# Optimization experiments

Measured on AMD Instinct MI355X. Metric: run time of the kernel, lower is better.

Reference implementation:

```python
import jax, jax.numpy as jnp
import numpy as np

V, H, L, NH, I, S, B, T = 30522, 768, 12, 12, 3072, 512, 16, 2
DH = H // NH
EPS = 1e-12


def layer_norm(x, w, b):
    u = x.mean(-1, keepdims=True)
    s = ((x - u) ** 2).mean(-1, keepdims=True)
    return w * (x - u) / jnp.sqrt(s + EPS) + b


def setup_inputs() -> dict:
    key = jax.random.key(0)
    ks = jax.random.split(key, 32)
    std = 0.02
    inp = {
        "input_ids": jax.random.randint(ks[0], (B, S), 0, V),
        "token_type_ids": jax.random.randint(ks[1], (B, S), 0, T),
        "attention_mask": jnp.ones((B, S), jnp.float32),
        "word_emb": std * jax.random.normal(ks[2], (V, H), jnp.float32),
        "pos_emb": std * jax.random.normal(ks[3], (S, H), jnp.float32),
        "type_emb": std * jax.random.normal(ks[4], (T, H), jnp.float32),
        "emb_ln_w": jnp.ones((H,), jnp.float32),
        "emb_ln_b": jnp.zeros((H,), jnp.float32),
        # stacked per-layer params, layout [L, in, out] for x @ W + b
        "Wq": std * jax.random.normal(ks[5], (L, H, H), jnp.float32),
        "bq": jnp.zeros((L, H), jnp.float32),
        "Wk": std * jax.random.normal(ks[6], (L, H, H), jnp.float32),
        "bk": jnp.zeros((L, H), jnp.float32),
        "Wv": std * jax.random.normal(ks[7], (L, H, H), jnp.float32),
        "bv": jnp.zeros((L, H), jnp.float32),
        "Wo": std * jax.random.normal(ks[8], (L, H, H), jnp.float32),
        "bo": jnp.zeros((L, H), jnp.float32),
        "ln1_w": jnp.ones((L, H), jnp.float32),
        "ln1_b": jnp.zeros((L, H), jnp.float32),
        "W1": std * jax.random.normal(ks[9], (L, H, I), jnp.float32),
        "b1": jnp.zeros((L, I), jnp.float32),
        "W2": std * jax.random.normal(ks[10], (L, I, H), jnp.float32),
        "b2": jnp.zeros((L, H), jnp.float32),
        "ln2_w": jnp.ones((L, H), jnp.float32),
        "ln2_b": jnp.zeros((L, H), jnp.float32),
    }
    return inp


def bert_forward(input_ids, token_type_ids, attention_mask,
                 word_emb, pos_emb, type_emb, emb_ln_w, emb_ln_b,
                 Wq, bq, Wk, bk, Wv, bv, Wo, bo, ln1_w, ln1_b,
                 W1, b1, W2, b2, ln2_w, ln2_b):
    b, s = input_ids.shape
    # extended attention mask: (1 - mask) * -10000, broadcast [B,1,1,S]
    ext_mask = ((1.0 - attention_mask) * -10000.0)[:, None, None, :]

    x = word_emb[input_ids] + pos_emb[None, :s] + type_emb[token_type_ids]
    x = layer_norm(x, emb_ln_w, emb_ln_b)  # [B,S,H]

    def block(h, p):
        (wq, bq_, wk, bk_, wv, bv_, wo, bo_, l1w, l1b, w1, b1_, w2, b2_, l2w, l2b) = p
        def heads(y):  # [B,S,H] -> [B,NH,S,DH]
            return y.reshape(b, s, NH, DH).transpose(0, 2, 1, 3)
        q = heads(h @ wq + bq_)
        k = heads(h @ wk + bk_)
        v = heads(h @ wv + bv_)
        scores = jnp.einsum("bhqd,bhkd->bhqk", q, k) / jnp.sqrt(jnp.float32(DH))
        scores = scores + ext_mask
        probs = jax.nn.softmax(scores, axis=-1)
        ctx = jnp.einsum("bhqk,bhkd->bhqd", probs, v)
        ctx = ctx.transpose(0, 2, 1, 3).reshape(b, s, H)
        attn_out = ctx @ wo + bo_
        h = layer_norm(attn_out + h, l1w, l1b)
        ffn = jax.nn.gelu(h @ w1 + b1_, approximate=False) @ w2 + b2_
        h = layer_norm(ffn + h, l2w, l2b)
        return h, None

    params = (Wq, bq, Wk, bk, Wv, bv, Wo, bo, ln1_w, ln1_b, W1, b1, W2, b2, ln2_w, ln2_b)
    x, _ = jax.lax.scan(block, x, params)
    return x


def reference(input_ids, token_type_ids, attention_mask,
              word_emb, pos_emb, type_emb, emb_ln_w, emb_ln_b,
              Wq, bq, Wk, bk, Wv, bv, Wo, bo, ln1_w, ln1_b,
              W1, b1, W2, b2, ln2_w, ln2_b):
    return bert_forward(input_ids, token_type_ids, attention_mask,
                        word_emb, pos_emb, type_emb, emb_ln_w, emb_ln_b,
                        Wq, bq, Wk, bk, Wv, bv, Wo, bo, ln1_w, ln1_b,
                        W1, b1, W2, b2, ln2_w, ln2_b)
```

## Files before the change

### kernel.cpp

```cpp
#include <hip/hip_runtime.h>
#include <math.h>

typedef unsigned short u16;
typedef __bf16 bf16x8 __attribute__((ext_vector_type(8)));
typedef float f32x4 __attribute__((ext_vector_type(4)));
typedef unsigned short u16x8 __attribute__((ext_vector_type(8)));

__device__ __forceinline__ u16 f2b(float f) {
    union { float f; unsigned int u; } v; v.f = f;
    unsigned int u = v.u;
    u += 0x7fffu + ((u >> 16) & 1u);
    return (u16)(u >> 16);
}

__device__ __forceinline__ f32x4 mfma16(bf16x8 a, bf16x8 b, f32x4 c) {
    return __builtin_amdgcn_mfma_f32_16x16x32_bf16(a, b, c, 0, 0, 0);
}

__device__ __forceinline__ void g2l16(const u16* g, const u16* l) {
    __builtin_amdgcn_global_load_lds(
        reinterpret_cast<const __attribute__((address_space(1))) unsigned int*>(
            reinterpret_cast<uintptr_t>(g)),
        reinterpret_cast<__attribute__((address_space(3))) unsigned int*>(
            reinterpret_cast<uintptr_t>(l)),
        16, 0, 0);
}

__global__ __launch_bounds__(256) void transpose_all(
    const float* __restrict__ Wq, const float* __restrict__ Wk,
    const float* __restrict__ Wv, const float* __restrict__ Wo,
    const float* __restrict__ W1, const float* __restrict__ W2,
    u16* __restrict__ out) {
    int bid = blockIdx.x;
    int layer = bid / 1728;
    int w = bid % 1728;
    const float* src; u16* dst; int K, N, tid;
    u16* lbase = out + (size_t)layer * 7077888;
    if (w < 576) {
        int m = w / 144; tid = w % 144; K = 768; N = 768;
        const float* s4[4] = {Wq, Wk, Wv, Wo};
        src = s4[m] + (size_t)layer * 589824;
        dst = lbase + (size_t)m * 589824;
    } else if (w < 1152) {
        tid = w - 576; K = 768; N = 3072;
        src = W1 + (size_t)layer * 2359296;
        dst = lbase + 2359296;
    } else {
        tid = w - 1152; K = 3072; N = 768;
        src = W2 + (size_t)layer * 2359296;
        dst = lbase + 4718592;
    }
    int ntn = N >> 6;
    int tk = tid / ntn, tn = tid % ntn;
    int k0 = tk << 6, n0 = tn << 6;
    __shared__ float tile[64][68];
    int t = threadIdx.x;
    int tx4 = (t & 15) * 4, r = t >> 4;
#pragma unroll
    for (int i = 0; i < 4; i++) {
        int row = r + i * 16;
        *(f32x4*)&tile[row][tx4] =
            *(const f32x4*)&src[(size_t)(k0 + row) * N + n0 + tx4];
    }
    __syncthreads();
#pragma unroll
    for (int i = 0; i < 2; i++) {
        int idx = t + i * 256;
        int n = idx & 63, kk = (idx >> 6) * 8;
        u16x8 o;
#pragma unroll
        for (int j = 0; j < 8; j++) o[j] = f2b(tile[kk + j][n]);
        *(u16x8*)&dst[(size_t)(n0 + n) * K + k0 + kk] = o;
    }
}

__global__ __launch_bounds__(256) void pack_bias(
    const float* __restrict__ bq, const float* __restrict__ bk,
    const float* __restrict__ bv, float* __restrict__ out) {
    int i = blockIdx.x * 256 + threadIdx.x;
    if (i < 12 * 2304) {
        int l = i / 2304, r = i % 2304;
        float v = (r < 768) ? bq[l * 768 + r]
                : (r < 1536) ? bk[l * 768 + r - 768]
                             : bv[l * 768 + r - 1536];
        out[i] = v;
    }
}

__device__ __forceinline__ void block_red2(float& a, float& b, float* red) {
#pragma unroll
    for (int mk = 1; mk < 64; mk <<= 1) {
        a += __shfl_xor(a, mk, 64);
        b += __shfl_xor(b, mk, 64);
    }
    int w = threadIdx.x >> 6;
    if ((threadIdx.x & 63) == 0) { red[w * 2] = a; red[w * 2 + 1] = b; }
    __syncthreads();
    a = red[0] + red[2] + red[4] + red[6];
    b = red[1] + red[3] + red[5] + red[7];
}

__global__ __launch_bounds__(256) void embed_ln(
    const int* __restrict__ ids, const int* __restrict__ tts,
    const float* __restrict__ we, const float* __restrict__ pe,
    const float* __restrict__ te, const float* __restrict__ lw,
    const float* __restrict__ lb, float* __restrict__ x, u16* __restrict__ xb) {
    int tok = blockIdx.x, t = threadIdx.x;
    int s = tok & 511;
    size_t wrow = (size_t)ids[tok] * 768;
    size_t trow = (size_t)tts[tok] * 768;
    __shared__ float red[8];
    float e[3], sum = 0.f, sq = 0.f;
#pragma unroll
    for (int i = 0; i < 3; i++) {
        int j = i * 256 + t;
        e[i] = we[wrow + j] + pe[(size_t)s * 768 + j] + te[trow + j];
        sum += e[i]; sq += e[i] * e[i];
    }
    block_red2(sum, sq, red);
    float u = sum * (1.0f / 768.0f);
    float var = sq * (1.0f / 768.0f) - u * u;
    float rs = rsqrtf(fmaxf(var, 0.0f) + 1e-12f);
#pragma unroll
    for (int i = 0; i < 3; i++) {
        int j = i * 256 + t;
        float o = lw[j] * ((e[i] - u) * rs) + lb[j];
        x[(size_t)tok * 768 + j] = o;
        xb[(size_t)tok * 768 + j] = f2b(o);
    }
}

template <int WRITE_XB>
__global__ __launch_bounds__(256) void add_ln2(
    const float* __restrict__ tin, const float* __restrict__ lw,
    const float* __restrict__ lb, float* __restrict__ xout,
    u16* __restrict__ xb) {
    int tok = blockIdx.x, t = threadIdx.x;
    __shared__ float red[8];
    float e[3], sum = 0.f, sq = 0.f;
#pragma unroll
    for (int i = 0; i < 3; i++) {
        int j = i * 256 + t;
        e[i] = tin[(size_t)tok * 768 + j];
        sum += e[i]; sq += e[i] * e[i];
    }
    block_red2(sum, sq, red);
    float u = sum * (1.0f / 768.0f);
    float var = sq * (1.0f / 768.0f) - u * u;
    float rs = rsqrtf(fmaxf(var, 0.0f) + 1e-12f);
#pragma unroll
    for (int i = 0; i < 3; i++) {
        int j = i * 256 + t;
        float o = lw[j] * ((e[i] - u) * rs) + lb[j];
        xout[(size_t)tok * 768 + j] = o;
        if (WRITE_XB) xb[(size_t)tok * 768 + j] = f2b(o);
    }
}

template <int EPI>
__global__ __launch_bounds__(256) void gemm_k(
    const u16* __restrict__ A, const u16* __restrict__ Bt,
    const float* __restrict__ bias, void* __restrict__ Cout,
    int M, int N, int K, const float* __restrict__ res) {
    __shared__ u16 As[128 * 32];
    __shared__ u16 Bs[128 * 32];
    int t = threadIdx.x;
    int w = t >> 6, lane = t & 63, quad = lane >> 4, l15 = lane & 15;
    int wr = (w >> 1) * 64, wc = (w & 1) * 64;
    int m0 = blockIdx.y * 128, n0 = blockIdx.x * 128;
    const u16* Ap = A + (size_t)m0 * K;
    const u16* Bp = Bt + (size_t)n0 * K;

    int sr = lane >> 2;
    int sc = (lane & 3) << 3;
    const u16* ag0 = Ap + (size_t)((w << 4) + sr) * K + sc;
    const u16* ag1 = Ap + (size_t)((w << 4) + 64 + sr) * K + sc;
    const u16* bg0 = Bp + (size_t)((w << 4) + sr) * K + sc;
    const u16* bg1 = Bp + (size_t)((w << 4) + 64 + sr) * K + sc;
    u16* al0 = As + (w << 4) * 32;
    u16* al1 = As + ((w << 4) + 64) * 32;
    u16* bl0 = Bs + (w << 4) * 32;
    u16* bl1 = Bs + ((w << 4) + 64) * 32;

    f32x4 acc[4][4];
#pragma unroll
    for (int i = 0; i < 4; i++)
#pragma unroll
        for (int j = 0; j < 4; j++) acc[i][j] = (f32x4){0.f, 0.f, 0.f, 0.f};

    for (int k0 = 0; k0 < K; k0 += 32) {
        g2l16(ag0 + k0, al0);
        g2l16(ag1 + k0, al1);
        g2l16(bg0 + k0, bl0);
        g2l16(bg1 + k0, bl1);
        __syncthreads();
        bf16x8 af[4], bf[4];
#pragma unroll
        for (int mi = 0; mi < 4; mi++)
            af[mi] = *(const bf16x8*)&As[(wr + mi * 16 + l15) * 32 + quad * 8];
#pragma unroll
        for (int ni = 0; ni < 4; ni++)
            bf[ni] = *(const bf16x8*)&Bs[(wc + ni * 16 + l15) * 32 + quad * 8];
#pragma unroll
        for (int mi = 0; mi < 4; mi++)
#pragma unroll
            for (int ni = 0; ni < 4; ni++)
                acc[mi][ni] = mfma16(af[mi], bf[ni], acc[mi][ni]);
        __syncthreads();
    }
#pragma unroll
    for (int mi = 0; mi < 4; mi++) {
#pragma unroll
        for (int ni = 0; ni < 4; ni++) {
            int cn = n0 + wc + ni * 16 + l15;
            float bb = bias[cn];
#pragma unroll
            for (int r = 0; r < 4; r++) {
                int cm = m0 + wr + mi * 16 + quad * 4 + r;
                float v = acc[mi][ni][r] + bb;
                if (EPI == 2) v = 0.5f * v * (1.0f + erff(v * 0.70710678118654752f));
                if (EPI == 3) {
                    v += res[(size_t)cm * N + cn];
                    ((float*)Cout)[(size_t)cm * N + cn] = v;
                } else if (EPI == 0)
                    ((float*)Cout)[(size_t)cm * N + cn] = v;
                else
                    ((u16*)Cout)[(size_t)cm * N + cn] = f2b(v);
            }
        }
    }
}

__global__ __launch_bounds__(256) void attn_k(
    const u16* __restrict__ qkv, const float* __restrict__ amask,
    u16* __restrict__ ctx) {
    int bid = blockIdx.x;
    int qt = bid & 7, h = (bid >> 3) % 12, b = bid / 96;
    __shared__ u16 Qs[64][72], Ks[64][72], Vs[64][72];
    __shared__ u16 Ps[4][16][72];
    __shared__ float em[512];
    int t = threadIdx.x, w = t >> 6, lane = t & 63, quad = lane >> 4, l15 = lane & 15;
    const int HQ = 2304;
    size_t rowbase = (size_t)(b * 512) * HQ + h * 64;
#pragma unroll
    for (int i = 0; i < 2; i++) {
        int c = t + i * 256, row = c >> 3, d0 = (c & 7) * 8;
        *(u16x8*)&Qs[row][d0] = *(const u16x8*)(qkv + rowbase + (size_t)(qt * 64 + row) * HQ + d0);
    }
    for (int j = t; j < 512; j += 256)
        em[j] = (1.0f - amask[b * 512 + j]) * -10000.0f;

#pragma unroll
    for (int i = 0; i < 2; i++) {
        int c = t + i * 256, row = c >> 3, d0 = (c & 7) * 8;
        size_t g = rowbase + (size_t)row * HQ + d0;
        *(u16x8*)&Ks[row][d0] = *(const u16x8*)(qkv + g + 768);
        u16x8 vv = *(const u16x8*)(qkv + g + 1536);
        int key = (c & 7) << 3;
#pragma unroll
        for (int j = 0; j < 8; j++) Vs[d0 + j][row ^ key] = vv[j];
    }
    u16x8 kq[2], vq[2];
#pragma unroll
    for (int i = 0; i < 2; i++) {
        int c = t + i * 256, row = c >> 3, d0 = (c & 7) * 8;
        size_t g = rowbase + (size_t)(64 + row) * HQ + d0;
        kq[i] = *(const u16x8*)(qkv + g + 768);
        vq[i] = *(const u16x8*)(qkv + g + 1536);
    }

    float m_run[4], l_run[4];
    f32x4 acc_o[4];
#pragma unroll
    for (int r = 0; r < 4; r++) { m_run[r] = -1e30f; l_run[r] = 0.0f; }
#pragma unroll
    for (int i = 0; i < 4; i++) acc_o[i] = (f32x4){0.f, 0.f, 0.f, 0.f};
    __syncthreads();

    for (int kt = 0; kt < 8; kt++) {
        f32x4 acc_s[4];
#pragma unroll
        for (int i = 0; i < 4; i++) acc_s[i] = (f32x4){0.f, 0.f, 0.f, 0.f};
#pragma unroll
        for (int ks = 0; ks < 2; ks++) {
            bf16x8 aq = *(const bf16x8*)&Qs[w * 16 + l15][ks * 32 + quad * 8];
#pragma unroll
            for (int nt = 0; nt < 4; nt++) {
                bf16x8 bk = *(const bf16x8*)&Ks[nt * 16 + l15][ks * 32 + quad * 8];
                acc_s[nt] = mfma16(aq, bk, acc_s[nt]);
            }
        }
        float tm[4] = {-3e38f, -3e38f, -3e38f, -3e38f};
#pragma unroll
        for (int nt = 0; nt < 4; nt++)
#pragma unroll
            for (int r = 0; r < 4; r++) {
                float sc = acc_s[nt][r] * 0.125f + em[kt * 64 + nt * 16 + l15];
                acc_s[nt][r] = sc;
                tm[r] = fmaxf(tm[r], sc);
            }
#pragma unroll
        for (int r = 0; r < 4; r++) {
#pragma unroll
            for (int mk = 1; mk < 16; mk <<= 1)
                tm[r] = fmaxf(tm[r], __shfl_xor(tm[r], mk, 64));
        }
        float al[4], ps[4];
#pragma unroll
        for (int r = 0; r < 4; r++) {
            float nm = fmaxf(m_run[r], tm[r]);
            al[r] = __expf(m_run[r] - nm);
            m_run[r] = nm;
            ps[r] = 0.0f;
        }
#pragma unroll
        for (int nt = 0; nt < 4; nt++)
#pragma unroll
            for (int r = 0; r < 4; r++) {
                float p = __expf(acc_s[nt][r] - m_run[r]);
                ps[r] += p;
                Ps[w][quad * 4 + r][nt * 16 + l15] = f2b(p);
            }
#pragma unroll
        for (int r = 0; r < 4; r++) {
#pragma unroll
            for (int mk = 1; mk < 16; mk <<= 1) ps[r] += __shfl_xor(ps[r], mk, 64);
            l_run[r] = l_run[r] * al[r] + ps[r];
#pragma unroll
            for (int nt = 0; nt < 4; nt++) acc_o[nt][r] *= al[r];
        }
        __syncthreads();
#pragma unroll
        for (int ks = 0; ks < 2; ks++) {
            bf16x8 ap = *(const bf16x8*)&Ps[w][l15][ks * 32 + quad * 8];
#pragma unroll
            for (int nt = 0; nt < 4; nt++) {
                int d = nt * 16 + l15;
                int key = ((d >> 3) & 7) << 3;
                bf16x8 bv = *(const bf16x8*)&Vs[d][(ks * 32 + quad * 8) ^ key];
                acc_o[nt] = mfma16(ap, bv, acc_o[nt]);
            }
        }
        __syncthreads();
        if (kt < 7) {
#pragma unroll
            for (int i = 0; i < 2; i++) {
                int c = t + i * 256, row = c >> 3, d0 = (c & 7) * 8;
                *(u16x8*)&Ks[row][d0] = kq[i];
                int key = (c & 7) << 3;
#pragma unroll
                for (int j = 0; j < 8; j++) Vs[d0 + j][row ^ key] = vq[i][j];
            }
            if (kt < 6) {
#pragma unroll
                for (int i = 0; i < 2; i++) {
                    int c = t + i * 256, row = c >> 3, d0 = (c & 7) * 8;
                    size_t g = rowbase + (size_t)((kt + 2) * 64 + row) * HQ + d0;
                    kq[i] = *(const u16x8*)(qkv + g + 768);
                    vq[i] = *(const u16x8*)(qkv + g + 1536);
                }
            }
            __syncthreads();
        }
    }
#pragma unroll
    for (int nt = 0; nt < 4; nt++)
#pragma unroll
        for (int r = 0; r < 4; r++) {
            int q = qt * 64 + w * 16 + quad * 4 + r;
            int d = nt * 16 + l15;
            ctx[(size_t)(b * 512 + q) * 768 + h * 64 + d] = f2b(acc_o[nt][r] / l_run[r]);
        }
}

extern "C" void kernel_launch(void* const* d_in, const int* in_sizes, int n_in,
                              void* d_out, int out_size, void* d_ws, size_t ws_size,
                              hipStream_t stream) {
    const int*   ids   = (const int*)d_in[0];
    const int*   tts   = (const int*)d_in[1];
    const float* amask = (const float*)d_in[2];
    const float* we    = (const float*)d_in[3];
    const float* pe    = (const float*)d_in[4];
    const float* te    = (const float*)d_in[5];
    const float* elw   = (const float*)d_in[6];
    const float* elb   = (const float*)d_in[7];
    const float* Wq    = (const float*)d_in[8];
    const float* bq    = (const float*)d_in[9];
    const float* Wk    = (const float*)d_in[10];
    const float* bk    = (const float*)d_in[11];
    const float* Wv    = (const float*)d_in[12];
    const float* bv    = (const float*)d_in[13];
    const float* Wo    = (const float*)d_in[14];
    const float* bo    = (const float*)d_in[15];
    const float* ln1w  = (const float*)d_in[16];
    const float* ln1b  = (const float*)d_in[17];
    const float* W1    = (const float*)d_in[18];
    const float* b1    = (const float*)d_in[19];
    const float* W2    = (const float*)d_in[20];
    const float* b2    = (const float*)d_in[21];
    const float* ln2w  = (const float*)d_in[22];
    const float* ln2b  = (const float*)d_in[23];

    char* base = (char*)d_ws;
    size_t off = 0;
    auto take = [&](size_t bytes) {
        char* r = base + off;
        off = (off + bytes + 255) & ~(size_t)255;
        return (void*)r;
    };
    u16*   wt   = (u16*)  take(169869312ULL);
    float* bqkv = (float*)take(110592ULL);
    float* x    = (float*)take(25165824ULL);
    float* tb   = (float*)take(25165824ULL);
    u16*   xb   = (u16*)  take(12582912ULL);
    u16*   qkvb = (u16*)  take(37748736ULL);
    u16*   ctxb = (u16*)  take(12582912ULL);
    u16*   midb = (u16*)  take(50331648ULL);
    (void)ws_size; (void)in_sizes; (void)n_in; (void)out_size;

    transpose_all<<<20736, 256, 0, stream>>>(Wq, Wk, Wv, Wo, W1, W2, wt);
    pack_bias<<<108, 256, 0, stream>>>(bq, bk, bv, bqkv);
    embed_ln<<<8192, 256, 0, stream>>>(ids, tts, we, pe, te, elw, elb, x, xb);

    for (int l = 0; l < 12; l++) {
        const u16* lw = wt + (size_t)l * 7077888;
        gemm_k<1><<<dim3(18, 64), 256, 0, stream>>>(xb, lw, bqkv + l * 2304, qkvb,
                                                    8192, 2304, 768, nullptr);
        attn_k<<<1536, 256, 0, stream>>>(qkvb, amask, ctxb);
        gemm_k<3><<<dim3(6, 64), 256, 0, stream>>>(ctxb, lw + 1769472, bo + l * 768, tb,
                                                   8192, 768, 768, x);
        add_ln2<1><<<8192, 256, 0, stream>>>(tb, ln1w + l * 768, ln1b + l * 768, x, xb);
        gemm_k<2><<<dim3(24, 64), 256, 0, stream>>>(xb, lw + 2359296, b1 + l * 3072, midb,
                                                    8192, 3072, 768, nullptr);
        gemm_k<3><<<dim3(6, 64), 256, 0, stream>>>(midb, lw + 4718592, b2 + l * 768, tb,
                                                   8192, 768, 3072, x);
        if (l < 11)
            add_ln2<1><<<8192, 256, 0, stream>>>(tb, ln2w + l * 768, ln2b + l * 768, x, xb);
        else
            add_ln2<0><<<8192, 256, 0, stream>>>(tb, ln2w + 11 * 768, ln2b + 11 * 768,
                                                 (float*)d_out, nullptr);
    }
}
```

Measured before the change: 4.175 ms.

## Replace GEMM with triple-buffered 128x192 pipelined kernel using swizzled LDS

Replaces the simple single-buffered GEMM with a 512-thread kernel that computes 128x192 tiles with K=64 stages. It triple-buffers LDS, uses an XOR-swizzled layout to avoid bank conflicts, and places manual barriers and vmcnt waits so global-to-LDS loads overlap MFMA work. The launch grid is remapped so groups of blocks share panels for L2 locality. The transpose kernel also switches to a padded scalar LDS tile with a different read mapping. The main aim is to hide memory latency and raise MFMA utilisation, at the cost of fragile hand-written synchronisation and a tile shape that must divide N.

New measurement: 3.505 ms. 1.19x faster.

```diff
diff --git a/kernel.cpp b/kernel.cpp
--- a/kernel.cpp
+++ b/kernel.cpp
@@ -25,6 +25,8 @@
             reinterpret_cast<uintptr_t>(l)),
         16, 0, 0);
 }
+
+#define BAR() asm volatile("s_barrier" ::: "memory")
 
 __global__ __launch_bounds__(256) void transpose_all(
     const float* __restrict__ Wq, const float* __restrict__ Wk,
@@ -53,24 +55,27 @@
     int ntn = N >> 6;
     int tk = tid / ntn, tn = tid % ntn;
     int k0 = tk << 6, n0 = tn << 6;
-    __shared__ float tile[64][68];
+    __shared__ float tile[64][65];
     int t = threadIdx.x;
-    int tx4 = (t & 15) * 4, r = t >> 4;
+    int tx4 = (t & 15) * 4, r4 = t >> 4;
 #pragma unroll
     for (int i = 0; i < 4; i++) {
-        int row = r + i * 16;
-        *(f32x4*)&tile[row][tx4] =
-            *(const f32x4*)&src[(size_t)(k0 + row) * N + n0 + tx4];
+        int row = r4 + i * 16;
+        f32x4 v = *(const f32x4*)&src[(size_t)(k0 + row) * N + n0 + tx4];
+        tile[row][tx4 + 0] = v[0];
+        tile[row][tx4 + 1] = v[1];
+        tile[row][tx4 + 2] = v[2];
+        tile[row][tx4 + 3] = v[3];
     }
     __syncthreads();
 #pragma unroll
     for (int i = 0; i < 2; i++) {
         int idx = t + i * 256;
-        int n = idx & 63, kk = (idx >> 6) * 8;
+        int n = idx >> 3, kk8 = (idx & 7) * 8;
         u16x8 o;
 #pragma unroll
-        for (int j = 0; j < 8; j++) o[j] = f2b(tile[kk + j][n]);
-        *(u16x8*)&dst[(size_t)(n0 + n) * K + k0 + kk] = o;
+        for (int j = 0; j < 8; j++) o[j] = f2b(tile[kk8 + j][n]);
+        *(u16x8*)&dst[(size_t)(n0 + n) * K + k0 + kk8] = o;
     }
 }
 
@@ -157,75 +162,134 @@
     }
 }
 
-template <int EPI>
-__global__ __launch_bounds__(256) void gemm_k(
+template <int EPI, int NKT>
+__global__ __launch_bounds__(512, 2) void gemm_p(
     const u16* __restrict__ A, const u16* __restrict__ Bt,
     const float* __restrict__ bias, void* __restrict__ Cout,
-    int M, int N, int K, const float* __restrict__ res) {
-    __shared__ u16 As[128 * 32];
-    __shared__ u16 Bs[128 * 32];
+    int N, const float* __restrict__ res) {
+    const int K = NKT * 64;
+    __shared__ u16 SA[3][128 * 64];
+    __shared__ u16 SB[3][192 * 64];
     int t = threadIdx.x;
-    int w = t >> 6, lane = t & 63, quad = lane >> 4, l15 = lane & 15;
-    int wr = (w >> 1) * 64, wc = (w & 1) * 64;
-    int m0 = blockIdx.y * 128, n0 = blockIdx.x * 128;
-    const u16* Ap = A + (size_t)m0 * K;
-    const u16* Bp = Bt + (size_t)n0 * K;
-
-    int sr = lane >> 2;
-    int sc = (lane & 3) << 3;
-    const u16* ag0 = Ap + (size_t)((w << 4) + sr) * K + sc;
-    const u16* ag1 = Ap + (size_t)((w << 4) + 64 + sr) * K + sc;
-    const u16* bg0 = Bp + (size_t)((w << 4) + sr) * K + sc;
-    const u16* bg1 = Bp + (size_t)((w << 4) + 64 + sr) * K + sc;
-    u16* al0 = As + (w << 4) * 32;
-    u16* al1 = As + ((w << 4) + 64) * 32;
-    u16* bl0 = Bs + (w << 4) * 32;
-    u16* bl1 = Bs + ((w << 4) + 64) * 32;
-
-    f32x4 acc[4][4];
+    int l = t & 63, w = t >> 6;
+    int l15 = l & 15, quad = l >> 4;
+    int wm = w >> 2, wn = w & 3;
+
+    int nwg = gridDim.x;
+    int lw = (blockIdx.x & 7) * (nwg >> 3) + (blockIdx.x >> 3);
+    int m0 = (lw & 63) << 7;
+    int n0 = (lw >> 6) * 192;
+
+    int cs8 = ((l & 7) ^ (l >> 3)) << 3;
+    const u16* sA0 = A + (size_t)(m0 + w * 16 + (l >> 3)) * K + cs8;
+    const u16* sA1 = sA0 + (size_t)8 * K;
+    const u16* sB0 = Bt + (size_t)(n0 + w * 24 + (l >> 3)) * K + cs8;
+    const u16* sB1 = sB0 + (size_t)8 * K;
+    const u16* sB2 = sB0 + (size_t)16 * K;
+    int aW = w * 1024;
+    int bW = w * 1536;
+
+    auto stage3 = [&](int kt, u16* sa, u16* sb) {
+        g2l16(sA0 + kt * 64, sa + aW);
+        g2l16(sA1 + kt * 64, sa + aW + 512);
+        g2l16(sB0 + kt * 64, sb + bW);
+    };
+    auto stage2 = [&](int kt, u16* sb) {
+        g2l16(sB1 + kt * 64, sb + bW + 512);
+        g2l16(sB2 + kt * 64, sb + bW + 1024);
+    };
+
+    int rA0 = (wm * 64 + 0 * 16 + l15) << 7;
+    int rA1 = (wm * 64 + 1 * 16 + l15) << 7;
+    int rA2 = (wm * 64 + 2 * 16 + l15) << 7;
+    int rA3 = (wm * 64 + 3 * 16 + l15) << 7;
+    int rB0 = (wn * 48 + 0 * 16 + l15) << 7;
+    int rB1 = (wn * 48 + 1 * 16 + l15) << 7;
+    int rB2 = (wn * 48 + 2 * 16 + l15) << 7;
+    int xk0 = ((quad ^ (l15 & 7)) << 4);
+    int xk1 = (((4 + quad) ^ (l15 & 7)) << 4);
+
+    f32x4 acc[4][3];
 #pragma unroll
     for (int i = 0; i < 4; i++)
 #pragma unroll
-        for (int j = 0; j < 4; j++) acc[i][j] = (f32x4){0.f, 0.f, 0.f, 0.f};
-
-    for (int k0 = 0; k0 < K; k0 += 32) {
-        g2l16(ag0 + k0, al0);
-        g2l16(ag1 + k0, al1);
-        g2l16(bg0 + k0, bl0);
-        g2l16(bg1 + k0, bl1);
-        __syncthreads();
-        bf16x8 af[4], bf[4];
-#pragma unroll
-        for (int mi = 0; mi < 4; mi++)
-            af[mi] = *(const bf16x8*)&As[(wr + mi * 16 + l15) * 32 + quad * 8];
-#pragma unroll
-        for (int ni = 0; ni < 4; ni++)
-            bf[ni] = *(const bf16x8*)&Bs[(wc + ni * 16 + l15) * 32 + quad * 8];
-#pragma unroll
-        for (int mi = 0; mi < 4; mi++)
-#pragma unroll
-            for (int ni = 0; ni < 4; ni++)
-                acc[mi][ni] = mfma16(af[mi], bf[ni], acc[mi][ni]);
-        __syncthreads();
-    }
+        for (int j = 0; j < 3; j++) acc[i][j] = (f32x4){0.f, 0.f, 0.f, 0.f};
+
+#define PHASE(sa_, sb_, xk_, ...)                                              \
+    {                                                                          \
+        bf16x8 af0 = *(const bf16x8*)((const char*)(sa_) + rA0 + (xk_));       \
+        bf16x8 af1 = *(const bf16x8*)((const char*)(sa_) + rA1 + (xk_));       \
+        bf16x8 af2 = *(const bf16x8*)((const char*)(sa_) + rA2 + (xk_));       \
+        bf16x8 af3 = *(const bf16x8*)((const char*)(sa_) + rA3 + (xk_));       \
+        bf16x8 bf0 = *(const bf16x8*)((const char*)(sb_) + rB0 + (xk_));       \
+        bf16x8 bf1 = *(const bf16x8*)((const char*)(sb_) + rB1 + (xk_));       \
+        bf16x8 bf2 = *(const bf16x8*)((const char*)(sb_) + rB2 + (xk_));       \
+        __VA_ARGS__;                                                           \
+        BAR();                                                                 \
+        asm volatile("s_waitcnt lgkmcnt(0)" ::: "memory");                     \
+        __builtin_amdgcn_sched_barrier(0);                                     \
+        __builtin_amdgcn_s_setprio(1);                                         \
+        acc[0][0] = mfma16(af0, bf0, acc[0][0]);                               \
+        acc[0][1] = mfma16(af0, bf1, acc[0][1]);                               \
+        acc[0][2] = mfma16(af0, bf2, acc[0][2]);                               \
+        acc[1][0] = mfma16(af1, bf0, acc[1][0]);                               \
+        acc[1][1] = mfma16(af1, bf1, acc[1][1]);                               \
+        acc[1][2] = mfma16(af1, bf2, acc[1][2]);                               \
+        acc[2][0] = mfma16(af2, bf0, acc[2][0]);                               \
+        acc[2][1] = mfma16(af2, bf1, acc[2][1]);                               \
+        acc[2][2] = mfma16(af2, bf2, acc[2][2]);                               \
+        acc[3][0] = mfma16(af3, bf0, acc[3][0]);                               \
+        acc[3][1] = mfma16(af3, bf1, acc[3][1]);                               \
+        acc[3][2] = mfma16(af3, bf2, acc[3][2]);                               \
+        __builtin_amdgcn_s_setprio(0);                                         \
+    }
+
+#define TILE(kt_, bR, bW2)                                                     \
+    {                                                                          \
+        const u16* sa = SA[bR]; const u16* sb = SB[bR];                        \
+        u16* wa = SA[bW2]; u16* wb = SB[bW2];                                  \
+        PHASE(sa, sb, xk0, if ((kt_) + 2 < NKT) stage3((kt_) + 2, wa, wb));    \
+        BAR();                                                                 \
+        PHASE(sa, sb, xk1, if ((kt_) + 2 < NKT) stage2((kt_) + 2, wb));        \
+        if ((kt_) <= NKT - 3) {                                                \
+            asm volatile("s_waitcnt vmcnt(5)" ::: "memory");                   \
+        } else if ((kt_) == NKT - 2) {                                         \
+            asm volatile("s_waitcnt vmcnt(0)" ::: "memory");                   \
+        }                                                                      \
+        BAR();                                                                 \
+    }
+
+    stage3(0, SA[0], SB[0]); stage2(0, SB[0]);
+    stage3(1, SA[1], SB[1]); stage2(1, SB[1]);
+    asm volatile("s_waitcnt vmcnt(5)" ::: "memory");
+    BAR();
+
+#pragma unroll 1
+    for (int kt = 0; kt < NKT; kt += 3) {
+        TILE(kt + 0, 0, 2);
+        TILE(kt + 1, 1, 0);
+        TILE(kt + 2, 2, 1);
+    }
+#undef PHASE
+#undef TILE
+
 #pragma unroll
     for (int mi = 0; mi < 4; mi++) {
 #pragma unroll
-        for (int ni = 0; ni < 4; ni++) {
-            int cn = n0 + wc + ni * 16 + l15;
+        for (int ni = 0; ni < 3; ni++) {
+            int cn = n0 + wn * 48 + ni * 16 + l15;
             float bb = bias[cn];
 #pragma unroll
             for (int r = 0; r < 4; r++) {
-                int cm = m0 + wr + mi * 16 + quad * 4 + r;
+                int cm = m0 + wm * 64 + mi * 16 + quad * 4 + r;
                 float v = acc[mi][ni][r] + bb;
                 if (EPI == 2) v = 0.5f * v * (1.0f + erff(v * 0.70710678118654752f));
                 if (EPI == 3) {
                     v += res[(size_t)cm * N + cn];
                     ((float*)Cout)[(size_t)cm * N + cn] = v;
-                } else if (EPI == 0)
-                    ((float*)Cout)[(size_t)cm * N + cn] = v;
-                else
+                } else {
                     ((u16*)Cout)[(size_t)cm * N + cn] = f2b(v);
+                }
             }
         }
     }
@@ -424,16 +488,16 @@
 
     for (int l = 0; l < 12; l++) {
         const u16* lw = wt + (size_t)l * 7077888;
-        gemm_k<1><<<dim3(18, 64), 256, 0, stream>>>(xb, lw, bqkv + l * 2304, qkvb,
-                                                    8192, 2304, 768, nullptr);
+        gemm_p<1, 12><<<768, 512, 0, stream>>>(xb, lw, bqkv + l * 2304, qkvb,
+                                               2304, nullptr);
         attn_k<<<1536, 256, 0, stream>>>(qkvb, amask, ctxb);
-        gemm_k<3><<<dim3(6, 64), 256, 0, stream>>>(ctxb, lw + 1769472, bo + l * 768, tb,
-                                                   8192, 768, 768, x);
+        gemm_p<3, 12><<<256, 512, 0, stream>>>(ctxb, lw + 1769472, bo + l * 768, tb,
+                                               768, x);
         add_ln2<1><<<8192, 256, 0, stream>>>(tb, ln1w + l * 768, ln1b + l * 768, x, xb);
-        gemm_k<2><<<dim3(24, 64), 256, 0, stream>>>(xb, lw + 2359296, b1 + l * 3072, midb,
-                                                    8192, 3072, 768, nullptr);
-        gemm_k<3><<<dim3(6, 64), 256, 0, stream>>>(midb, lw + 4718592, b2 + l * 768, tb,
-                                                   8192, 768, 3072, x);
+        gemm_p<2, 12><<<1024, 512, 0, stream>>>(xb, lw + 2359296, b1 + l * 3072, midb,
+                                                3072, nullptr);
+        gemm_p<3, 48><<<256, 512, 0, stream>>>(midb, lw + 4718592, b2 + l * 768, tb,
+                                               768, x);
         if (l < 11)
             add_ln2<1><<<8192, 256, 0, stream>>>(tb, ln2w + l * 768, ln2b + l * 768, x, xb);
         else
```
